# Performance work log

Hardware: AMD Instinct MI355X
Metric: run time of the kernel (lower is better)

## Reference

```python
import jax, jax.numpy as jnp
import numpy as np
from jax import lax

NEG_SLOPE = 0.2
BN_EPS = 1e-5


def _edges(n_nodes, n_total):
    # complete graph (no self loops) on the first n_nodes nodes, as in create_complete_graph,
    # plus PyG GATConv default add_self_loops over ALL n_total nodes.
    i = np.arange(n_nodes)
    src = np.repeat(i, n_nodes)
    dst = np.tile(i, n_nodes)
    keep = src != dst
    loops = np.arange(n_total)
    src = np.concatenate([src[keep], loops]).astype(np.int32)
    dst = np.concatenate([dst[keep], loops]).astype(np.int32)
    return jnp.asarray(src), jnp.asarray(dst)


def _bn_eval(x, g, b, m, v):
    # x: [B, C, H, W]; eval-mode batchnorm with running stats
    inv = g / jnp.sqrt(v + BN_EPS)
    return x * inv[None, :, None, None] + (b - m * inv)[None, :, None, None]


def _gat(x, W, a_src, a_dst, bias, src, dst, n_total):
    h = x @ W                      # [N, D_out]
    s = h @ a_src                  # [N] per-node source score
    d = h @ a_dst                  # [N] per-node dest score
    e = jax.nn.leaky_relu(s[src] + d[dst], NEG_SLOPE)          # [E]
    emax = jax.ops.segment_max(e, dst, num_segments=n_total)   # [N]
    ex = jnp.exp(e - emax[dst])
    denom = jax.ops.segment_sum(ex, dst, num_segments=n_total)
    alpha = ex / denom[dst]                                    # [E]
    out = jax.ops.segment_sum(alpha[:, None] * h[src], dst, num_segments=n_total)
    return out + bias


def setup_inputs() -> dict:
    key = jax.random.key(0)
    ks = jax.random.split(key, 12)
    B, H, W = 8, 64, 64

    def rn(k, shape, s):
        return jax.random.normal(k, shape, jnp.float32) * s

    return {
        "images": jax.random.normal(ks[0], (B, 3, H, W), jnp.float32),
        "conv1_w": rn(ks[1], (64, 3, 3, 3), 0.1), "conv1_b": jnp.zeros((64,), jnp.float32),
        "bn1_g": jnp.ones((64,), jnp.float32), "bn1_b": jnp.zeros((64,), jnp.float32),
        "bn1_m": jnp.zeros((64,), jnp.float32), "bn1_v": jnp.ones((64,), jnp.float32),
        "conv2_w": rn(ks[2], (128, 64, 3, 3), 0.05), "conv2_b": jnp.zeros((128,), jnp.float32),
        "bn2_g": jnp.ones((128,), jnp.float32), "bn2_b": jnp.zeros((128,), jnp.float32),
        "bn2_m": jnp.zeros((128,), jnp.float32), "bn2_v": jnp.ones((128,), jnp.float32),
        "gat1_w": rn(ks[3], (128, 256), 0.05), "gat1_asrc": rn(ks[4], (256,), 0.05),
        "gat1_adst": rn(ks[5], (256,), 0.05), "gat1_bias": jnp.zeros((256,), jnp.float32),
        "gat2_w": rn(ks[6], (256, 128), 0.05), "gat2_asrc": rn(ks[7], (128,), 0.05),
        "gat2_adst": rn(ks[8], (128,), 0.05), "gat2_bias": jnp.zeros((128,), jnp.float32),
        "out_w": rn(ks[9], (128, 10), 0.05), "out_b": jnp.zeros((10,), jnp.float32),
    }


def reference(images, conv1_w, conv1_b, bn1_g, bn1_b, bn1_m, bn1_v,
              conv2_w, conv2_b, bn2_g, bn2_b, bn2_m, bn2_v,
              gat1_w, gat1_asrc, gat1_adst, gat1_bias,
              gat2_w, gat2_asrc, gat2_adst, gat2_bias,
              out_w, out_b):
    dn = ("NCHW", "OIHW", "NCHW")
    x = lax.conv_general_dilated(images, conv1_w, (1, 1), "SAME", dimension_numbers=dn)
    x = x + conv1_b[None, :, None, None]
    x = jax.nn.relu(_bn_eval(x, bn1_g, bn1_b, bn1_m, bn1_v))
    x = lax.reduce_window(x, -jnp.inf, lax.max, (1, 1, 2, 2), (1, 1, 2, 2), "VALID")
    x = lax.conv_general_dilated(x, conv2_w, (1, 1), "SAME", dimension_numbers=dn)
    x = x + conv2_b[None, :, None, None]
    x = jax.nn.relu(_bn_eval(x, bn2_g, bn2_b, bn2_m, bn2_v))

    B = x.shape[0]
    n_nodes = x.shape[2] * x.shape[3]          # (H/2)*(W/2) = 1024
    x = x.reshape(B, 128, n_nodes).transpose(0, 2, 1).reshape(-1, 128)  # [B*n, 128]
    n_total = B * n_nodes
    src, dst = _edges(n_nodes, n_total)

    x = jax.nn.relu(_gat(x, gat1_w, gat1_asrc, gat1_adst, gat1_bias, src, dst, n_total))
    x = jax.nn.relu(_gat(x, gat2_w, gat2_asrc, gat2_adst, gat2_bias, src, dst, n_total))

    x = x.reshape(B, n_nodes, 128).mean(axis=1)   # global_mean_pool over each image's nodes
    logits = x @ out_w + out_b
    return jax.nn.log_softmax(logits, axis=1)
```

## Files before the change

kernel.cpp:

```cpp
#include <hip/hip_runtime.h>
#include <math.h>

#define BN_EPS 1e-5f
#define NEG_SLOPE 0.2f

__device__ __forceinline__ float relu_f(float x) { return x > 0.f ? x : 0.f; }
__device__ __forceinline__ float leaky_f(float z) { return z > 0.f ? z : NEG_SLOPE * z; }

__global__ void conv1_pool(const float* __restrict__ img, const float* __restrict__ w,
                           const float* __restrict__ cb, const float* __restrict__ g,
                           const float* __restrict__ bb, const float* __restrict__ m,
                           const float* __restrict__ vv, float* __restrict__ out)
{
    int blk = blockIdx.x;
    int q = blk & 3, cog = (blk >> 2) & 15, b = blk >> 6;
    int t = threadIdx.x;
    int x = t & 31, y = (q << 3) + (t >> 5);

    float acc[4][4] = {};
#pragma unroll
    for (int ci = 0; ci < 3; ++ci) {
        const float* ib = img + (b * 3 + ci) * 4096;
        float rv[4][4];
#pragma unroll
        for (int r = 0; r < 4; ++r) {
            int yy = 2 * y - 1 + r;
            bool yok = (unsigned)yy < 64u;
            const float* p = ib + yy * 64 + 2 * x;
            float2 c01 = yok ? *(const float2*)p : make_float2(0.f, 0.f);
            rv[r][1] = c01.x;
            rv[r][2] = c01.y;
            rv[r][0] = (yok && x > 0) ? p[-1] : 0.f;
            rv[r][3] = (yok && x < 31) ? p[2] : 0.f;
        }
#pragma unroll
        for (int j = 0; j < 4; ++j) {
            const float* wj = w + ((cog * 4 + j) * 3 + ci) * 9;
#pragma unroll
            for (int ky = 0; ky < 3; ++ky)
#pragma unroll
                for (int kx = 0; kx < 3; ++kx) {
                    float wvv = wj[ky * 3 + kx];
#pragma unroll
                    for (int py = 0; py < 2; ++py)
#pragma unroll
                        for (int px = 0; px < 2; ++px)
                            acc[j][py * 2 + px] += rv[py + ky][px + kx] * wvv;
                }
        }
    }
#pragma unroll
    for (int j = 0; j < 4; ++j) {
        int co = cog * 4 + j;
        float inv = g[co] / sqrtf(vv[co] + BN_EPS);
        float sh = cb[co] * inv + (bb[co] - m[co] * inv);
        float v0 = relu_f(acc[j][0] * inv + sh);
        float v1 = relu_f(acc[j][1] * inv + sh);
        float v2 = relu_f(acc[j][2] * inv + sh);
        float v3 = relu_f(acc[j][3] * inv + sh);
        out[((b * 64 + co) * 32 + y) * 32 + x] = fmaxf(fmaxf(v0, v1), fmaxf(v2, v3));
    }
}

__global__ void conv2_fused(const float* __restrict__ in, const float* __restrict__ w,
                            const float* __restrict__ cb, const float* __restrict__ g,
                            const float* __restrict__ bb, const float* __restrict__ m,
                            const float* __restrict__ vv, float* __restrict__ x0)
{
    int blk = blockIdx.x;
    int half = blk & 1, cog = (blk >> 1) & 31, b = blk >> 6;
    int t = threadIdx.x;
    int x2p = (t & 15) * 2;
    int y = half * 16 + (t >> 4);
    bool xnz = x2p != 0;
    bool xhi = x2p == 30;
    const float* ibase = in + b * 64 * 1024;
    int xb = xnz ? x2p - 1 : 0;

    float acc[4][2] = {};

#pragma unroll 2
    for (int ci = 0; ci < 64; ++ci) {
        const float* cb2 = ibase + ci * 1024;
        float rc[3][4];
#pragma unroll
        for (int r = 0; r < 3; ++r) {
            int yy = y - 1 + r;
            bool yok = (unsigned)yy < 32u;
            const float* p = cb2 + yy * 32 + xb;
            float4 f = yok ? *(const float4*)p : make_float4(0.f, 0.f, 0.f, 0.f);
            rc[r][0] = xnz ? f.x : 0.f;
            rc[r][1] = xnz ? f.y : f.x;
            rc[r][2] = xnz ? f.z : f.y;
            float r3 = xnz ? f.w : f.z;
            rc[r][3] = xhi ? 0.f : r3;
        }
#pragma unroll
        for (int j = 0; j < 4; ++j) {
            const float* wj = w + ((cog * 4 + j) * 64 + ci) * 9;
#pragma unroll
            for (int ky = 0; ky < 3; ++ky)
#pragma unroll
                for (int kx = 0; kx < 3; ++kx) {
                    float wvv = wj[ky * 3 + kx];
                    acc[j][0] += rc[ky][kx] * wvv;
                    acc[j][1] += rc[ky][kx + 1] * wvv;
                }
        }
    }

    float o0[4], o1[4];
#pragma unroll
    for (int j = 0; j < 4; ++j) {
        int co = cog * 4 + j;
        float inv = g[co] / sqrtf(vv[co] + BN_EPS);
        float sh = cb[co] * inv + (bb[co] - m[co] * inv);
        o0[j] = relu_f(acc[j][0] * inv + sh);
        o1[j] = relu_f(acc[j][1] * inv + sh);
    }
    int n0 = b * 1024 + y * 32 + x2p;
    float4 s0 = {o0[0], o0[1], o0[2], o0[3]};
    float4 s1 = {o1[0], o1[1], o1[2], o1[3]};
    *(float4*)&x0[(size_t)n0 * 128 + cog * 4] = s0;
    *(float4*)&x0[(size_t)(n0 + 1) * 128 + cog * 4] = s1;
}

template <int K, int N>
__global__ void gemm32(const float* __restrict__ A, const float* __restrict__ B,
                       float* __restrict__ C)
{
    __shared__ float As[16][32];
    __shared__ float Bs[16][64];
    int t = threadIdx.x;
    int m0 = blockIdx.x * 32;
    int n0 = blockIdx.y * 64;
    int tx = t & 15, ty = t >> 4;
    int am = t >> 2, akq = (t & 3) * 4;
    float acc[4][4] = {};

    for (int k0 = 0; k0 < K; k0 += 16) {
        float4 av = *(const float4*)&A[(size_t)(m0 + am) * K + k0 + akq];
        float4 bv0 = *(const float4*)&B[(size_t)(k0 + ty) * N + n0 + tx * 4];
        float4 bv1 = *(const float4*)&B[(size_t)(k0 + 8 + ty) * N + n0 + tx * 4];
        __syncthreads();
        As[akq + 0][am] = av.x;
        As[akq + 1][am] = av.y;
        As[akq + 2][am] = av.z;
        As[akq + 3][am] = av.w;
        *(float4*)&Bs[ty][tx * 4] = bv0;
        *(float4*)&Bs[ty + 8][tx * 4] = bv1;
        __syncthreads();
#pragma unroll
        for (int kk = 0; kk < 16; ++kk) {
            float4 a4 = *(const float4*)&As[kk][ty * 4];
            float4 b4 = *(const float4*)&Bs[kk][tx * 4];
            float aa[4] = {a4.x, a4.y, a4.z, a4.w};
            float bb4[4] = {b4.x, b4.y, b4.z, b4.w};
#pragma unroll
            for (int i = 0; i < 4; ++i)
#pragma unroll
                for (int j = 0; j < 4; ++j)
                    acc[i][j] += aa[i] * bb4[j];
        }
    }
#pragma unroll
    for (int i = 0; i < 4; ++i) {
        float4 o = {acc[i][0], acc[i][1], acc[i][2], acc[i][3]};
        *(float4*)&C[(size_t)(m0 + ty * 4 + i) * N + n0 + tx * 4] = o;
    }
}

__global__ void score_kernel(const float* __restrict__ h, const float* __restrict__ asrc,
                             const float* __restrict__ adst, float* __restrict__ s,
                             float* __restrict__ d, int D, int N)
{
    int gt = blockIdx.x * blockDim.x + threadIdx.x;
    int wave = gt >> 6, lane = gt & 63;
    if (wave >= N) return;
    const float* hp = h + (size_t)wave * D;
    float ss = 0.f, dd = 0.f;
    for (int c = lane; c < D; c += 64) {
        float hv = hp[c];
        ss += hv * asrc[c];
        dd += hv * adst[c];
    }
    for (int off = 32; off; off >>= 1) {
        ss += __shfl_down(ss, off);
        dd += __shfl_down(dd, off);
    }
    if (lane == 0) { s[wave] = ss; d[wave] = dd; }
}

template <int D, int KS>
__global__ void gat_agg_gemm(const float* __restrict__ h, const float* __restrict__ s,
                             const float* __restrict__ d, float* __restrict__ pacc,
                             float* __restrict__ pden)
{
    __shared__ float Ss[1024];
    __shared__ float As[16][32];
    __shared__ float Bs[16][64];
    __shared__ float red[2];
    __shared__ float part[16][32];

    const int CH = 1024 / KS;
    int t = threadIdx.x;
    int m0 = blockIdx.x * 32;
    int n0 = blockIdx.y * 64;
    int kz = blockIdx.z;
    int tx = t & 15, ty = t >> 4;
    int ug = t >> 3, vg4 = (t & 7) * 4;

    float4 sa = *(const float4*)&s[t * 8];
    float4 sb = *(const float4*)&s[t * 8 + 4];
    *(float4*)&Ss[t * 8] = sa;
    *(float4*)&Ss[t * 8 + 4] = sb;
    float lm = fmaxf(fmaxf(fmaxf(sa.x, sa.y), fmaxf(sa.z, sa.w)),
                     fmaxf(fmaxf(sb.x, sb.y), fmaxf(sb.z, sb.w)));
#pragma unroll
    for (int off = 1; off < 64; off <<= 1) lm = fmaxf(lm, __shfl_xor(lm, off));
    if ((t & 63) == 0) red[t >> 6] = lm;
    __syncthreads();
    float smax = fmaxf(red[0], red[1]);

    float4 dv = *(const float4*)&d[m0 + vg4];
    float4 mv = {leaky_f(smax + dv.x), leaky_f(smax + dv.y),
                 leaky_f(smax + dv.z), leaky_f(smax + dv.w)};
    float4 dsum = {0.f, 0.f, 0.f, 0.f};
    float acc[4][4] = {};

    for (int k0 = kz * CH; k0 < kz * CH + CH; k0 += 16) {
        float4 bv0 = *(const float4*)&h[(size_t)(k0 + ty) * D + n0 + tx * 4];
        float4 bv1 = *(const float4*)&h[(size_t)(k0 + 8 + ty) * D + n0 + tx * 4];
        float su = Ss[k0 + ug];
        float4 avv;
        avv.x = __expf(leaky_f(su + dv.x) - mv.x);
        avv.y = __expf(leaky_f(su + dv.y) - mv.y);
        avv.z = __expf(leaky_f(su + dv.z) - mv.z);
        avv.w = __expf(leaky_f(su + dv.w) - mv.w);
        dsum.x += avv.x; dsum.y += avv.y; dsum.z += avv.z; dsum.w += avv.w;
        __syncthreads();
        *(float4*)&As[ug][vg4] = avv;
        *(float4*)&Bs[ty][tx * 4] = bv0;
        *(float4*)&Bs[ty + 8][tx * 4] = bv1;
        __syncthreads();
#pragma unroll
        for (int kk = 0; kk < 16; ++kk) {
            float4 a4 = *(const float4*)&As[kk][ty * 4];
            float4 b4 = *(const float4*)&Bs[kk][tx * 4];
            float aa[4] = {a4.x, a4.y, a4.z, a4.w};
            float bb4[4] = {b4.x, b4.y, b4.z, b4.w};
#pragma unroll
            for (int i = 0; i < 4; ++i)
#pragma unroll
                for (int j = 0; j < 4; ++j)
                    acc[i][j] += aa[i] * bb4[j];
        }
    }

    __syncthreads();
    *(float4*)&part[ug][vg4] = dsum;
    __syncthreads();

#pragma unroll
    for (int i = 0; i < 4; ++i) {
        int r = ty * 4 + i;
        float4 o = {acc[i][0], acc[i][1], acc[i][2], acc[i][3]};
        *(float4*)&pacc[((size_t)kz * 1024 + m0 + r) * D + n0 + tx * 4] = o;
    }
    if (t < 32) {
        float den = 0.f;
#pragma unroll
        for (int u = 0; u < 16; ++u) den += part[u][t];
        pden[kz * 1024 + m0 + t] = den;
    }
}

template <int D, int KS>
__global__ void gat_combine(const float* __restrict__ pacc, const float* __restrict__ pden,
                            const float* __restrict__ bias, float* __restrict__ out)
{
    int idx = blockIdx.x * blockDim.x + threadIdx.x;
    if (idx >= 1024 * D / 4) return;
    int c4 = idx & (D / 4 - 1);
    int v = idx / (D / 4);
    float4 a = {0.f, 0.f, 0.f, 0.f};
    float den = 0.f;
#pragma unroll
    for (int ks = 0; ks < KS; ++ks) {
        float4 p = ((const float4*)pacc)[(size_t)(ks * 1024 + v) * (D / 4) + c4];
        a.x += p.x; a.y += p.y; a.z += p.z; a.w += p.w;
        den += pden[ks * 1024 + v];
    }
    float rd = 1.f / den;
    float4 bz = ((const float4*)bias)[c4];
    float4 o = {relu_f(a.x * rd + bz.x), relu_f(a.y * rd + bz.y),
                relu_f(a.z * rd + bz.z), relu_f(a.w * rd + bz.w)};
    ((float4*)out)[(size_t)v * (D / 4) + c4] = o;
}

template <int D>
__global__ void gat_self4(const float* __restrict__ h, const float* __restrict__ bias,
                          float* __restrict__ out)
{
    int idx = blockIdx.x * blockDim.x + threadIdx.x;
    if (idx >= 7168 * D / 4) return;
    int c4 = idx & (D / 4 - 1);
    int n = 1024 + idx / (D / 4);
    float4 v = ((const float4*)h)[(size_t)n * (D / 4) + c4];
    float4 bz = ((const float4*)bias)[c4];
    float4 o = {relu_f(v.x + bz.x), relu_f(v.y + bz.y),
                relu_f(v.z + bz.z), relu_f(v.w + bz.w)};
    ((float4*)out)[(size_t)n * (D / 4) + c4] = o;
}

__global__ void pool_part(const float* __restrict__ x2, float* __restrict__ part)
{
    int b = blockIdx.x >> 4, seg = blockIdx.x & 15, t = threadIdx.x;
    const float* p = x2 + ((size_t)b * 1024 + seg * 64) * 128 + t;
    float acc = 0.f;
#pragma unroll 8
    for (int n = 0; n < 64; ++n) acc += p[(size_t)n * 128];
    part[(b * 16 + seg) * 128 + t] = acc;
}

__global__ void head_kernel(const float* __restrict__ part, const float* __restrict__ ow,
                            const float* __restrict__ ob, float* __restrict__ out)
{
    __shared__ float pooled[128];
    __shared__ float logits[10];
    int b = blockIdx.x, t = threadIdx.x;
    float acc = 0.f;
#pragma unroll
    for (int sgi = 0; sgi < 16; ++sgi) acc += part[(b * 16 + sgi) * 128 + t];
    pooled[t] = acc * (1.f / 1024.f);
    __syncthreads();
    if (t < 10) {
        float l = ob[t];
        for (int c = 0; c < 128; ++c) l += pooled[c] * ow[c * 10 + t];
        logits[t] = l;
    }
    __syncthreads();
    if (t == 0) {
        float mx = logits[0];
        for (int j = 1; j < 10; ++j) mx = fmaxf(mx, logits[j]);
        float sum = 0.f;
        for (int j = 0; j < 10; ++j) sum += expf(logits[j] - mx);
        float lse = mx + logf(sum);
        for (int j = 0; j < 10; ++j) out[b * 10 + j] = logits[j] - lse;
    }
}

extern "C" void kernel_launch(void* const* d_in, const int* in_sizes, int n_in,
                              void* d_out, int out_size, void* d_ws, size_t ws_size,
                              hipStream_t stream)
{
    const float* images = (const float*)d_in[0];
    const float* c1w = (const float*)d_in[1];
    const float* c1b = (const float*)d_in[2];
    const float* bn1g = (const float*)d_in[3];
    const float* bn1b = (const float*)d_in[4];
    const float* bn1m = (const float*)d_in[5];
    const float* bn1v = (const float*)d_in[6];
    const float* c2w = (const float*)d_in[7];
    const float* c2b = (const float*)d_in[8];
    const float* bn2g = (const float*)d_in[9];
    const float* bn2b = (const float*)d_in[10];
    const float* bn2m = (const float*)d_in[11];
    const float* bn2v = (const float*)d_in[12];
    const float* g1w = (const float*)d_in[13];
    const float* g1as = (const float*)d_in[14];
    const float* g1ad = (const float*)d_in[15];
    const float* g1b = (const float*)d_in[16];
    const float* g2w = (const float*)d_in[17];
    const float* g2as = (const float*)d_in[18];
    const float* g2ad = (const float*)d_in[19];
    const float* g2b = (const float*)d_in[20];
    const float* ow = (const float*)d_in[21];
    const float* ob = (const float*)d_in[22];
    float* out = (float*)d_out;

    float* ws = (float*)d_ws;
    float* x1    = ws;
    float* bufc1 = ws + 2097152;
    float* h1    = ws + 2621440;
    float* x0    = ws + 4718592;
    float* h2    = ws + 5767168;
    float* s1    = ws + 6815744;
    float* d1    = ws + 6816768;
    float* s2    = ws + 6817792;
    float* d2    = ws + 6818816;
    float* part  = bufc1;
    float* pden1 = bufc1 + 16384;
    float* pden2 = bufc1 + 24576;
    float* pacc1 = x0;
    float* pacc2 = h1;
    float* x2    = x0;

    conv1_pool<<<512, 256, 0, stream>>>(images, c1w, c1b, bn1g, bn1b, bn1m, bn1v, bufc1);
    conv2_fused<<<512, 256, 0, stream>>>(bufc1, c2w, c2b, bn2g, bn2b, bn2m, bn2v, x0);

    gemm32<128, 256><<<dim3(256, 4), 128, 0, stream>>>(x0, g1w, h1);
    score_kernel<<<256, 256, 0, stream>>>(h1, g1as, g1ad, s1, d1, 256, 1024);
    gat_agg_gemm<256, 8><<<dim3(32, 4, 8), 128, 0, stream>>>(h1, s1, d1, pacc1, pden1);
    gat_combine<256, 8><<<256, 256, 0, stream>>>(pacc1, pden1, g1b, x1);
    gat_self4<256><<<1792, 256, 0, stream>>>(h1, g1b, x1);

    gemm32<256, 128><<<dim3(256, 2), 128, 0, stream>>>(x1, g2w, h2);
    score_kernel<<<256, 256, 0, stream>>>(h2, g2as, g2ad, s2, d2, 128, 1024);
    gat_agg_gemm<128, 16><<<dim3(32, 2, 16), 128, 0, stream>>>(h2, s2, d2, pacc2, pden2);
    gat_combine<128, 16><<<128, 256, 0, stream>>>(pacc2, pden2, g2b, x2);
    gat_self4<128><<<896, 256, 0, stream>>>(h2, g2b, x2);

    pool_part<<<128, 128, 0, stream>>>(x2, part);
    head_kernel<<<8, 128, 0, stream>>>(part, ow, ob, out);
}
```

Baseline: 217.4 us.

## Move GAT GEMMs and aggregation to bf16x3 split MFMA with transposed h

Result: slower. 240.0 us (+10.4%).

```diff
diff --git a/kernel.cpp b/kernel.cpp
--- a/kernel.cpp
+++ b/kernel.cpp
@@ -4,8 +4,25 @@
 #define BN_EPS 1e-5f
 #define NEG_SLOPE 0.2f
 
+typedef __attribute__((ext_vector_type(8))) short bf16x8;
+typedef __attribute__((ext_vector_type(4))) float f32x4;
+
 __device__ __forceinline__ float relu_f(float x) { return x > 0.f ? x : 0.f; }
 __device__ __forceinline__ float leaky_f(float z) { return z > 0.f ? z : NEG_SLOPE * z; }
+
+__device__ __forceinline__ unsigned short f2b(float f) {
+    union { float f; unsigned int i; } u; u.f = f;
+    unsigned int r = u.i + 0x7fffu + ((u.i >> 16) & 1u);
+    return (unsigned short)(r >> 16);
+}
+__device__ __forceinline__ float b2f(unsigned short v) {
+    union { unsigned int i; float f; } u; u.i = ((unsigned int)v) << 16;
+    return u.f;
+}
+__device__ __forceinline__ void split_b(float x, unsigned short& hi, unsigned short& lo) {
+    hi = f2b(x);
+    lo = f2b(x - b2f(hi));
+}
 
 __global__ void conv1_pool(const float* __restrict__ img, const float* __restrict__ w,
                            const float* __restrict__ cb, const float* __restrict__ g,
@@ -125,192 +142,281 @@
     *(float4*)&x0[(size_t)(n0 + 1) * 128 + cog * 4] = s1;
 }
 
-template <int K, int N>
-__global__ void gemm32(const float* __restrict__ A, const float* __restrict__ B,
-                       float* __restrict__ C)
-{
-    __shared__ float As[16][32];
-    __shared__ float Bs[16][64];
-    int t = threadIdx.x;
-    int m0 = blockIdx.x * 32;
-    int n0 = blockIdx.y * 64;
-    int tx = t & 15, ty = t >> 4;
-    int am = t >> 2, akq = (t & 3) * 4;
-    float acc[4][4] = {};
-
-    for (int k0 = 0; k0 < K; k0 += 16) {
-        float4 av = *(const float4*)&A[(size_t)(m0 + am) * K + k0 + akq];
-        float4 bv0 = *(const float4*)&B[(size_t)(k0 + ty) * N + n0 + tx * 4];
-        float4 bv1 = *(const float4*)&B[(size_t)(k0 + 8 + ty) * N + n0 + tx * 4];
+__global__ void wprep_w(const float* __restrict__ W1, const float* __restrict__ W2,
+                        unsigned short* __restrict__ W1H, unsigned short* __restrict__ W1L,
+                        unsigned short* __restrict__ W2H, unsigned short* __restrict__ W2L)
+{
+    int idx = blockIdx.x * 256 + threadIdx.x;
+    if (idx < 32768) {
+        int k = idx & 127, n = idx >> 7;
+        split_b(W1[k * 256 + n], W1H[idx], W1L[idx]);
+    } else {
+        int i = idx - 32768;
+        int k = i & 255, n = i >> 8;
+        split_b(W2[k * 128 + n], W2H[i], W2L[i]);
+    }
+}
+
+__global__ void xprep(const float* __restrict__ x0, unsigned short* __restrict__ xH,
+                      unsigned short* __restrict__ xL)
+{
+    int idx = blockIdx.x * 256 + threadIdx.x;
+    float4 v = ((const float4*)x0)[idx];
+    ushort4 h, l;
+    split_b(v.x, h.x, l.x);
+    split_b(v.y, h.y, l.y);
+    split_b(v.z, h.z, l.z);
+    split_b(v.w, h.w, l.w);
+    ((ushort4*)xH)[idx] = h;
+    ((ushort4*)xL)[idx] = l;
+}
+
+template <int K, int NN, int WRITE_T>
+__global__ void gemm_mfma(const unsigned short* __restrict__ AH, const unsigned short* __restrict__ AL,
+                          const unsigned short* __restrict__ BH, const unsigned short* __restrict__ BL,
+                          float* __restrict__ C, unsigned short* __restrict__ CTH,
+                          unsigned short* __restrict__ CTL)
+{
+    __shared__ short AsH[64][40], AsL[64][40];
+    __shared__ short BsH[64][40], BsL[64][40];
+    int t = threadIdx.x, w = t >> 6, l = t & 63;
+    int m0 = blockIdx.x * 64, n0 = blockIdx.y * 64;
+    int sm = t >> 2, sk8 = (t & 3) * 8;
+    f32x4 acc[4] = {};
+    for (int k0 = 0; k0 < K; k0 += 32) {
+        size_t ao = (size_t)(m0 + sm) * K + k0 + sk8;
+        size_t bo = (size_t)(n0 + sm) * K + k0 + sk8;
+        uint4 avh = *(const uint4*)&AH[ao];
+        uint4 avl = *(const uint4*)&AL[ao];
+        uint4 bvh = *(const uint4*)&BH[bo];
+        uint4 bvl = *(const uint4*)&BL[bo];
         __syncthreads();
-        As[akq + 0][am] = av.x;
-        As[akq + 1][am] = av.y;
-        As[akq + 2][am] = av.z;
-        As[akq + 3][am] = av.w;
-        *(float4*)&Bs[ty][tx * 4] = bv0;
-        *(float4*)&Bs[ty + 8][tx * 4] = bv1;
+        *(uint4*)&AsH[sm][sk8] = avh;
+        *(uint4*)&AsL[sm][sk8] = avl;
+        *(uint4*)&BsH[sm][sk8] = bvh;
+        *(uint4*)&BsL[sm][sk8] = bvl;
         __syncthreads();
-#pragma unroll
-        for (int kk = 0; kk < 16; ++kk) {
-            float4 a4 = *(const float4*)&As[kk][ty * 4];
-            float4 b4 = *(const float4*)&Bs[kk][tx * 4];
-            float aa[4] = {a4.x, a4.y, a4.z, a4.w};
-            float bb4[4] = {b4.x, b4.y, b4.z, b4.w};
-#pragma unroll
-            for (int i = 0; i < 4; ++i)
-#pragma unroll
-                for (int j = 0; j < 4; ++j)
-                    acc[i][j] += aa[i] * bb4[j];
-        }
-    }
-#pragma unroll
-    for (int i = 0; i < 4; ++i) {
-        float4 o = {acc[i][0], acc[i][1], acc[i][2], acc[i][3]};
-        *(float4*)&C[(size_t)(m0 + ty * 4 + i) * N + n0 + tx * 4] = o;
+        int ar = w * 16 + (l & 15), akk = (l >> 4) * 8;
+        bf16x8 afh = *(const bf16x8*)&AsH[ar][akk];
+        bf16x8 afl = *(const bf16x8*)&AsL[ar][akk];
+#pragma unroll
+        for (int nt = 0; nt < 4; ++nt) {
+            int br = nt * 16 + (l & 15);
+            bf16x8 bh = *(const bf16x8*)&BsH[br][akk];
+            bf16x8 bl = *(const bf16x8*)&BsL[br][akk];
+            acc[nt] = __builtin_amdgcn_mfma_f32_16x16x32_bf16(afh, bh, acc[nt], 0, 0, 0);
+            acc[nt] = __builtin_amdgcn_mfma_f32_16x16x32_bf16(afh, bl, acc[nt], 0, 0, 0);
+            acc[nt] = __builtin_amdgcn_mfma_f32_16x16x32_bf16(afl, bh, acc[nt], 0, 0, 0);
+        }
+    }
+    int rb = m0 + w * 16 + (l >> 4) * 4;
+#pragma unroll
+    for (int nt = 0; nt < 4; ++nt) {
+        int col = n0 + nt * 16 + (l & 15);
+        C[(size_t)(rb + 0) * NN + col] = acc[nt][0];
+        C[(size_t)(rb + 1) * NN + col] = acc[nt][1];
+        C[(size_t)(rb + 2) * NN + col] = acc[nt][2];
+        C[(size_t)(rb + 3) * NN + col] = acc[nt][3];
+        if (WRITE_T && rb < 1024) {
+            ushort4 ch, cl;
+            unsigned short hh, ll;
+            split_b(acc[nt][0], hh, ll); ch.x = hh; cl.x = ll;
+            split_b(acc[nt][1], hh, ll); ch.y = hh; cl.y = ll;
+            split_b(acc[nt][2], hh, ll); ch.z = hh; cl.z = ll;
+            split_b(acc[nt][3], hh, ll); ch.w = hh; cl.w = ll;
+            *(ushort4*)&CTH[(size_t)col * 1024 + rb] = ch;
+            *(ushort4*)&CTL[(size_t)col * 1024 + rb] = cl;
+        }
     }
 }
 
 __global__ void score_kernel(const float* __restrict__ h, const float* __restrict__ asrc,
                              const float* __restrict__ adst, float* __restrict__ s,
-                             float* __restrict__ d, int D, int N)
+                             float* __restrict__ d, int D)
 {
     int gt = blockIdx.x * blockDim.x + threadIdx.x;
-    int wave = gt >> 6, lane = gt & 63;
-    if (wave >= N) return;
-    const float* hp = h + (size_t)wave * D;
+    int row = gt >> 6, lane = gt & 63;
+    const float* hp = h + (size_t)row * D;
     float ss = 0.f, dd = 0.f;
-    for (int c = lane; c < D; c += 64) {
-        float hv = hp[c];
-        ss += hv * asrc[c];
-        dd += hv * adst[c];
+    for (int c0 = lane * 4; c0 < D; c0 += 256) {
+        float4 hv = *(const float4*)&hp[c0];
+        float4 a4 = *(const float4*)&asrc[c0];
+        float4 d4 = *(const float4*)&adst[c0];
+        ss += hv.x * a4.x + hv.y * a4.y + hv.z * a4.z + hv.w * a4.w;
+        dd += hv.x * d4.x + hv.y * d4.y + hv.z * d4.z + hv.w * d4.w;
     }
     for (int off = 32; off; off >>= 1) {
         ss += __shfl_down(ss, off);
         dd += __shfl_down(dd, off);
     }
-    if (lane == 0) { s[wave] = ss; d[wave] = dd; }
-}
-
-template <int D, int KS>
-__global__ void gat_agg_gemm(const float* __restrict__ h, const float* __restrict__ s,
-                             const float* __restrict__ d, float* __restrict__ pacc,
-                             float* __restrict__ pden)
-{
-    __shared__ float Ss[1024];
-    __shared__ float As[16][32];
-    __shared__ float Bs[16][64];
-    __shared__ float red[2];
-    __shared__ float part[16][32];
-
-    const int CH = 1024 / KS;
-    int t = threadIdx.x;
+    if (lane == 0) { s[row] = ss; d[row] = dd; }
+}
+
+template <int D>
+__global__ void gat_mfma(const unsigned short* __restrict__ hTH, const unsigned short* __restrict__ hTL,
+                         const float* __restrict__ s, const float* __restrict__ d,
+                         float* __restrict__ pacc, float* __restrict__ pden)
+{
+    constexpr int NT = D / 64;
+    __shared__ float Ss[128];
+    __shared__ short AsH[32][40], AsL[32][40];
+    __shared__ short BsH[D][40], BsL[D][40];
+    __shared__ float red[8][32];
+    __shared__ float red2[4];
+    int t = threadIdx.x, w = t >> 6, l = t & 63;
     int m0 = blockIdx.x * 32;
-    int n0 = blockIdx.y * 64;
-    int kz = blockIdx.z;
-    int tx = t & 15, ty = t >> 4;
-    int ug = t >> 3, vg4 = (t & 7) * 4;
-
-    float4 sa = *(const float4*)&s[t * 8];
-    float4 sb = *(const float4*)&s[t * 8 + 4];
-    *(float4*)&Ss[t * 8] = sa;
-    *(float4*)&Ss[t * 8 + 4] = sb;
-    float lm = fmaxf(fmaxf(fmaxf(sa.x, sa.y), fmaxf(sa.z, sa.w)),
-                     fmaxf(fmaxf(sb.x, sb.y), fmaxf(sb.z, sb.w)));
+    int kz = blockIdx.y;
+    int ub = kz << 7;
+
+    float4 sv = *(const float4*)&s[t * 4];
+    float lm = fmaxf(fmaxf(sv.x, sv.y), fmaxf(sv.z, sv.w));
 #pragma unroll
     for (int off = 1; off < 64; off <<= 1) lm = fmaxf(lm, __shfl_xor(lm, off));
-    if ((t & 63) == 0) red[t >> 6] = lm;
+    if (l == 0) red2[w] = lm;
+    if (t < 128) Ss[t] = s[ub + t];
     __syncthreads();
-    float smax = fmaxf(red[0], red[1]);
-
-    float4 dv = *(const float4*)&d[m0 + vg4];
-    float4 mv = {leaky_f(smax + dv.x), leaky_f(smax + dv.y),
-                 leaky_f(smax + dv.z), leaky_f(smax + dv.w)};
-    float4 dsum = {0.f, 0.f, 0.f, 0.f};
-    float acc[4][4] = {};
-
-    for (int k0 = kz * CH; k0 < kz * CH + CH; k0 += 16) {
-        float4 bv0 = *(const float4*)&h[(size_t)(k0 + ty) * D + n0 + tx * 4];
-        float4 bv1 = *(const float4*)&h[(size_t)(k0 + 8 + ty) * D + n0 + tx * 4];
-        float su = Ss[k0 + ug];
-        float4 avv;
-        avv.x = __expf(leaky_f(su + dv.x) - mv.x);
-        avv.y = __expf(leaky_f(su + dv.y) - mv.y);
-        avv.z = __expf(leaky_f(su + dv.z) - mv.z);
-        avv.w = __expf(leaky_f(su + dv.w) - mv.w);
-        dsum.x += avv.x; dsum.y += avv.y; dsum.z += avv.z; dsum.w += avv.w;
+    float smax = fmaxf(fmaxf(red2[0], red2[1]), fmaxf(red2[2], red2[3]));
+
+    int vv = t & 31, ug = t >> 5;
+    float dv = d[m0 + vv];
+    float mv = leaky_f(smax + dv);
+    float dsum = 0.f;
+    f32x4 acc[2][NT] = {};
+
+    for (int st = 0; st < 4; ++st) {
+        int u0l = st * 32;
+        ushort4 a4h, a4l;
+        unsigned short hh, ll;
+        float a0 = __expf(leaky_f(Ss[u0l + ug * 4 + 0] + dv) - mv);
+        float a1 = __expf(leaky_f(Ss[u0l + ug * 4 + 1] + dv) - mv);
+        float a2 = __expf(leaky_f(Ss[u0l + ug * 4 + 2] + dv) - mv);
+        float a3 = __expf(leaky_f(Ss[u0l + ug * 4 + 3] + dv) - mv);
+        dsum += a0 + a1 + a2 + a3;
+        split_b(a0, hh, ll); a4h.x = hh; a4l.x = ll;
+        split_b(a1, hh, ll); a4h.y = hh; a4l.y = ll;
+        split_b(a2, hh, ll); a4h.z = hh; a4l.z = ll;
+        split_b(a3, hh, ll); a4h.w = hh; a4l.w = ll;
+        uint4 bvh[NT], bvl[NT];
+#pragma unroll
+        for (int c = 0; c < NT; ++c) {
+            int chunk = c * 256 + t;
+            int n = chunk >> 2, kq8 = (chunk & 3) * 8;
+            size_t o = (size_t)n * 1024 + ub + u0l + kq8;
+            bvh[c] = *(const uint4*)&hTH[o];
+            bvl[c] = *(const uint4*)&hTL[o];
+        }
         __syncthreads();
-        *(float4*)&As[ug][vg4] = avv;
-        *(float4*)&Bs[ty][tx * 4] = bv0;
-        *(float4*)&Bs[ty + 8][tx * 4] = bv1;
+        *(ushort4*)&AsH[vv][ug * 4] = a4h;
+        *(ushort4*)&AsL[vv][ug * 4] = a4l;
+#pragma unroll
+        for (int c = 0; c < NT; ++c) {
+            int chunk = c * 256 + t;
+            int n = chunk >> 2, kq8 = (chunk & 3) * 8;
+            *(uint4*)&BsH[n][kq8] = bvh[c];
+            *(uint4*)&BsL[n][kq8] = bvl[c];
+        }
         __syncthreads();
-#pragma unroll
-        for (int kk = 0; kk < 16; ++kk) {
-            float4 a4 = *(const float4*)&As[kk][ty * 4];
-            float4 b4 = *(const float4*)&Bs[kk][tx * 4];
-            float aa[4] = {a4.x, a4.y, a4.z, a4.w};
-            float bb4[4] = {b4.x, b4.y, b4.z, b4.w};
-#pragma unroll
-            for (int i = 0; i < 4; ++i)
-#pragma unroll
-                for (int j = 0; j < 4; ++j)
-                    acc[i][j] += aa[i] * bb4[j];
-        }
-    }
-
+        int ar = l & 15, akk = (l >> 4) * 8;
+        bf16x8 af0h = *(const bf16x8*)&AsH[ar][akk];
+        bf16x8 af0l = *(const bf16x8*)&AsL[ar][akk];
+        bf16x8 af1h = *(const bf16x8*)&AsH[16 + ar][akk];
+        bf16x8 af1l = *(const bf16x8*)&AsL[16 + ar][akk];
+#pragma unroll
+        for (int nt = 0; nt < NT; ++nt) {
+            int br = w * (D / 4) + nt * 16 + ar;
+            bf16x8 bh = *(const bf16x8*)&BsH[br][akk];
+            bf16x8 bl = *(const bf16x8*)&BsL[br][akk];
+            acc[0][nt] = __builtin_amdgcn_mfma_f32_16x16x32_bf16(af0h, bh, acc[0][nt], 0, 0, 0);
+            acc[0][nt] = __builtin_amdgcn_mfma_f32_16x16x32_bf16(af0h, bl, acc[0][nt], 0, 0, 0);
+            acc[0][nt] = __builtin_amdgcn_mfma_f32_16x16x32_bf16(af0l, bh, acc[0][nt], 0, 0, 0);
+            acc[1][nt] = __builtin_amdgcn_mfma_f32_16x16x32_bf16(af1h, bh, acc[1][nt], 0, 0, 0);
+            acc[1][nt] = __builtin_amdgcn_mfma_f32_16x16x32_bf16(af1h, bl, acc[1][nt], 0, 0, 0);
+            acc[1][nt] = __builtin_amdgcn_mfma_f32_16x16x32_bf16(af1l, bh, acc[1][nt], 0, 0, 0);
+        }
+    }
     __syncthreads();
-    *(float4*)&part[ug][vg4] = dsum;
+    red[ug][vv] = dsum;
     __syncthreads();
-
-#pragma unroll
-    for (int i = 0; i < 4; ++i) {
-        int r = ty * 4 + i;
-        float4 o = {acc[i][0], acc[i][1], acc[i][2], acc[i][3]};
-        *(float4*)&pacc[((size_t)kz * 1024 + m0 + r) * D + n0 + tx * 4] = o;
-    }
     if (t < 32) {
-        float den = 0.f;
-#pragma unroll
-        for (int u = 0; u < 16; ++u) den += part[u][t];
-        pden[kz * 1024 + m0 + t] = den;
-    }
-}
-
-template <int D, int KS>
-__global__ void gat_combine(const float* __restrict__ pacc, const float* __restrict__ pden,
-                            const float* __restrict__ bias, float* __restrict__ out)
-{
-    int idx = blockIdx.x * blockDim.x + threadIdx.x;
-    if (idx >= 1024 * D / 4) return;
-    int c4 = idx & (D / 4 - 1);
-    int v = idx / (D / 4);
-    float4 a = {0.f, 0.f, 0.f, 0.f};
-    float den = 0.f;
-#pragma unroll
-    for (int ks = 0; ks < KS; ++ks) {
-        float4 p = ((const float4*)pacc)[(size_t)(ks * 1024 + v) * (D / 4) + c4];
-        a.x += p.x; a.y += p.y; a.z += p.z; a.w += p.w;
-        den += pden[ks * 1024 + v];
-    }
-    float rd = 1.f / den;
+        float dn = 0.f;
+#pragma unroll
+        for (int i = 0; i < 8; ++i) dn += red[i][t];
+        pden[(kz << 10) + m0 + t] = dn;
+    }
+    int rb = (l >> 4) * 4;
+#pragma unroll
+    for (int nt = 0; nt < NT; ++nt) {
+        int col = w * (D / 4) + nt * 16 + (l & 15);
+#pragma unroll
+        for (int mt = 0; mt < 2; ++mt)
+#pragma unroll
+            for (int r = 0; r < 4; ++r) {
+                int row = m0 + mt * 16 + rb + r;
+                pacc[((size_t)(kz << 10) + row) * D + col] = acc[mt][nt][r];
+            }
+    }
+}
+
+template <int D, int KS, int CLOG>
+__global__ void gat_fin_hl(const float* __restrict__ pacc, const float* __restrict__ pden,
+                           const float* __restrict__ h, const float* __restrict__ bias,
+                           unsigned short* __restrict__ outH, unsigned short* __restrict__ outL)
+{
+    int idx = blockIdx.x * 256 + threadIdx.x;
+    int c4 = idx & ((D / 4) - 1);
+    int v = idx >> CLOG;
     float4 bz = ((const float4*)bias)[c4];
-    float4 o = {relu_f(a.x * rd + bz.x), relu_f(a.y * rd + bz.y),
-                relu_f(a.z * rd + bz.z), relu_f(a.w * rd + bz.w)};
+    float vx, vy, vz, vw;
+    if (v < 1024) {
+        float ax = 0.f, ay = 0.f, az = 0.f, aw = 0.f, den = 0.f;
+#pragma unroll
+        for (int ks = 0; ks < KS; ++ks) {
+            float4 p = ((const float4*)pacc)[(size_t)((ks << 10) + v) * (D / 4) + c4];
+            ax += p.x; ay += p.y; az += p.z; aw += p.w;
+            den += pden[(ks << 10) + v];
+        }
+        float rd = 1.f / den;
+        vx = ax * rd; vy = ay * rd; vz = az * rd; vw = aw * rd;
+    } else {
+        float4 hv = *(const float4*)&h[(size_t)v * D + c4 * 4];
+        vx = hv.x; vy = hv.y; vz = hv.z; vw = hv.w;
+    }
+    ushort4 oh, ol;
+    unsigned short hh, ll;
+    split_b(relu_f(vx + bz.x), hh, ll); oh.x = hh; ol.x = ll;
+    split_b(relu_f(vy + bz.y), hh, ll); oh.y = hh; ol.y = ll;
+    split_b(relu_f(vz + bz.z), hh, ll); oh.z = hh; ol.z = ll;
+    split_b(relu_f(vw + bz.w), hh, ll); oh.w = hh; ol.w = ll;
+    *(ushort4*)&outH[(size_t)v * D + c4 * 4] = oh;
+    *(ushort4*)&outL[(size_t)v * D + c4 * 4] = ol;
+}
+
+template <int D, int KS, int CLOG>
+__global__ void gat_fin_f(const float* __restrict__ pacc, const float* __restrict__ pden,
+                          const float* __restrict__ h, const float* __restrict__ bias,
+                          float* __restrict__ out)
+{
+    int idx = blockIdx.x * 256 + threadIdx.x;
+    int c4 = idx & ((D / 4) - 1);
+    int v = idx >> CLOG;
+    float4 bz = ((const float4*)bias)[c4];
+    float vx, vy, vz, vw;
+    if (v < 1024) {
+        float ax = 0.f, ay = 0.f, az = 0.f, aw = 0.f, den = 0.f;
+#pragma unroll
+        for (int ks = 0; ks < KS; ++ks) {
+            float4 p = ((const float4*)pacc)[(size_t)((ks << 10) + v) * (D / 4) + c4];
+            ax += p.x; ay += p.y; az += p.z; aw += p.w;
+            den += pden[(ks << 10) + v];
+        }
+        float rd = 1.f / den;
+        vx = ax * rd; vy = ay * rd; vz = az * rd; vw = aw * rd;
+    } else {
+        float4 hv = *(const float4*)&h[(size_t)v * D + c4 * 4];
+        vx = hv.x; vy = hv.y; vz = hv.z; vw = hv.w;
+    }
+    float4 o = {relu_f(vx + bz.x), relu_f(vy + bz.y), relu_f(vz + bz.z), relu_f(vw + bz.w)};
     ((float4*)out)[(size_t)v * (D / 4) + c4] = o;
-}
-
-template <int D>
-__global__ void gat_self4(const float* __restrict__ h, const float* __restrict__ bias,
-                          float* __restrict__ out)
-{
-    int idx = blockIdx.x * blockDim.x + threadIdx.x;
-    if (idx >= 7168 * D / 4) return;
-    int c4 = idx & (D / 4 - 1);
-    int n = 1024 + idx / (D / 4);
-    float4 v = ((const float4*)h)[(size_t)n * (D / 4) + c4];
-    float4 bz = ((const float4*)bias)[c4];
-    float4 o = {relu_f(v.x + bz.x), relu_f(v.y + bz.y),
-                relu_f(v.z + bz.z), relu_f(v.w + bz.w)};
-    ((float4*)out)[(size_t)n * (D / 4) + c4] = o;
 }
 
 __global__ void pool_part(const float* __restrict__ x2, float* __restrict__ part)
@@ -379,37 +485,46 @@
     const float* ob = (const float*)d_in[22];
     float* out = (float*)d_out;
 
-    float* ws = (float*)d_ws;
-    float* x1    = ws;
-    float* bufc1 = ws + 2097152;
-    float* h1    = ws + 2621440;
-    float* x0    = ws + 4718592;
-    float* h2    = ws + 5767168;
-    float* s1    = ws + 6815744;
-    float* d1    = ws + 6816768;
-    float* s2    = ws + 6817792;
-    float* d2    = ws + 6818816;
-    float* part  = bufc1;
-    float* pden1 = bufc1 + 16384;
-    float* pden2 = bufc1 + 24576;
-    float* pacc1 = x0;
-    float* pacc2 = h1;
-    float* x2    = x0;
+    char* base = (char*)d_ws;
+    float*          h1    = (float*)(base + 0);
+    float*          h2    = (float*)(base + 0);
+    float*          pacc2 = (float*)(base + 4194304);
+    float*          bufc1 = (float*)(base + 8388608);
+    float*          x0f   = (float*)(base + 10485760);
+    unsigned short* x0H   = (unsigned short*)(base + 14680064);
+    unsigned short* x0L   = (unsigned short*)(base + 16777216);
+    float*          pacc1 = (float*)(base + 8388608);
+    float*          x2    = (float*)(base + 8388608);
+    unsigned short* x1H   = (unsigned short*)(base + 16777216);
+    unsigned short* x1L   = (unsigned short*)(base + 20971520);
+    unsigned short* hTH   = (unsigned short*)(base + 25165824);
+    unsigned short* hTL   = (unsigned short*)(base + 25690112);
+    unsigned short* W1H   = (unsigned short*)(base + 26214400);
+    unsigned short* W1L   = (unsigned short*)(base + 26279936);
+    unsigned short* W2H   = (unsigned short*)(base + 26345472);
+    unsigned short* W2L   = (unsigned short*)(base + 26411008);
+    float*          s1    = (float*)(base + 26542080);
+    float*          d1    = (float*)(base + 26546176);
+    float*          s2    = (float*)(base + 26550272);
+    float*          d2    = (float*)(base + 26554368);
+    float*          pden1 = (float*)(base + 26558464);
+    float*          pden2 = (float*)(base + 26591232);
+    float*          part  = (float*)(base + 26624000);
 
     conv1_pool<<<512, 256, 0, stream>>>(images, c1w, c1b, bn1g, bn1b, bn1m, bn1v, bufc1);
-    conv2_fused<<<512, 256, 0, stream>>>(bufc1, c2w, c2b, bn2g, bn2b, bn2m, bn2v, x0);
-
-    gemm32<128, 256><<<dim3(256, 4), 128, 0, stream>>>(x0, g1w, h1);
-    score_kernel<<<256, 256, 0, stream>>>(h1, g1as, g1ad, s1, d1, 256, 1024);
-    gat_agg_gemm<256, 8><<<dim3(32, 4, 8), 128, 0, stream>>>(h1, s1, d1, pacc1, pden1);
-    gat_combine<256, 8><<<256, 256, 0, stream>>>(pacc1, pden1, g1b, x1);
-    gat_self4<256><<<1792, 256, 0, stream>>>(h1, g1b, x1);
-
-    gemm32<256, 128><<<dim3(256, 2), 128, 0, stream>>>(x1, g2w, h2);
-    score_kernel<<<256, 256, 0, stream>>>(h2, g2as, g2ad, s2, d2, 128, 1024);
-    gat_agg_gemm<128, 16><<<dim3(32, 2, 16), 128, 0, stream>>>(h2, s2, d2, pacc2, pden2);
-    gat_combine<128, 16><<<128, 256, 0, stream>>>(pacc2, pden2, g2b, x2);
-    gat_self4<128><<<896, 256, 0, stream>>>(h2, g2b, x2);
+    conv2_fused<<<512, 256, 0, stream>>>(bufc1, c2w, c2b, bn2g, bn2b, bn2m, bn2v, x0f);
+    wprep_w<<<256, 256, 0, stream>>>(g1w, g2w, W1H, W1L, W2H, W2L);
+    xprep<<<1024, 256, 0, stream>>>(x0f, x0H, x0L);
+
+    gemm_mfma<128, 256, 1><<<dim3(128, 4), 256, 0, stream>>>(x0H, x0L, W1H, W1L, h1, hTH, hTL);
+    score_kernel<<<256, 256, 0, stream>>>(h1, g1as, g1ad, s1, d1, 256);
+    gat_mfma<256><<<dim3(32, 8), 256, 0, stream>>>(hTH, hTL, s1, d1, pacc1, pden1);
+    gat_fin_hl<256, 8, 6><<<2048, 256, 0, stream>>>(pacc1, pden1, h1, g1b, x1H, x1L);
+
+    gemm_mfma<256, 128, 1><<<dim3(128, 2), 256, 0, stream>>>(x1H, x1L, W2H, W2L, h2, hTH, hTL);
+    score_kernel<<<256, 256, 0, stream>>>(h2, g2as, g2ad, s2, d2, 128);
+    gat_mfma<128><<<dim3(32, 8), 256, 0, stream>>>(hTH, hTL, s2, d2, pacc2, pden2);
+    gat_fin_f<128, 8, 5><<<1024, 256, 0, stream>>>(pacc2, pden2, h2, g2b, x2);
 
     pool_part<<<128, 128, 0, stream>>>(x2, part);
     head_kernel<<<8, 128, 0, stream>>>(part, ow, ob, out);
```
